# Kernel optimization log

Measured on AMD Instinct MI355X. Metric: run time of the kernel, lower is better.

Reference implementation:

```python
import jax, jax.numpy as jnp
import numpy as np
from functools import partial

B, C, FD, H, W = 8, 256, 128, 64, 64
POSC = 34  # 32 learned pos channels + 2 raw meshgrid channels


def create_meshgrid(h, w):
    # kornia-style normalized grid in [-1, 1], returned as [1, 2, h, w] (x, y)
    xs = jnp.linspace(-1.0, 1.0, w, dtype=jnp.float32)
    ys = jnp.linspace(-1.0, 1.0, h, dtype=jnp.float32)
    gy, gx = jnp.meshgrid(ys, xs, indexing='ij')
    return jnp.stack([gx, gy], axis=0)[None]  # [1,2,h,w]


def conv1x1(x, w, b):
    return jnp.einsum('bchw,oc->bohw', x, w) + b[None, :, None, None]


def pos_gen(feat, pg_w1, pg_b1, pg_w2, pg_b2):
    # PosGen type=2 with detach: two 1x1 'mul' layers (conv + ReLU, no norm)
    b, c, h, w = feat.shape
    feat = jax.lax.stop_gradient(feat)
    pos = jnp.broadcast_to(create_meshgrid(h, w), (b, 2, h, w))
    inp = jnp.concatenate([pos + 1.0, feat], axis=1)           # [b, feat_dim+2, h, w]
    h1 = jax.nn.relu(conv1x1(inp, pg_w1, pg_b1))               # [b, feat_dim, h, w]
    h2 = jax.nn.relu(conv1x1(h1, pg_w2, pg_b2))                # [b, 32, h, w]
    return jnp.concatenate([h2, pos], axis=1)                  # [b, 34, h, w]


def fuser(x, feat, w1, b1, w2, b2):
    # fuser_1D: concat along channels, 1x1 -> hidden (ReLU) -> 1x1 -> 256
    z = jnp.concatenate([x, feat], axis=1)
    z = jax.nn.relu(conv1x1(z, w1, b1))
    return conv1x1(z, w2, b2)


def conv_y(y, dw_w, dw_b, pw_w, pw_b):
    # BasicDWLayer: depthwise 3x3 + pointwise 1x1, no norm, no activation
    z = jax.lax.conv_general_dilated(
        y, dw_w, window_strides=(1, 1), padding='SAME',
        feature_group_count=y.shape[1],
        dimension_numbers=('NCHW', 'OIHW', 'NCHW')) + dw_b[None, :, None, None]
    return conv1x1(z, pw_w, pw_b)


def matching_forward(x, y, feat1, feat2,
                     pg_w1, pg_b1, pg_w2, pg_b2,
                     fus_w1, fus_b1, fus_w2, fus_b2,
                     dw_w, dw_b, pw_w, pw_b,
                     dustbin_vec, dustbin_pos):
    b, c, hx, wx = x.shape
    hy, wy = y.shape[2], y.shape[3]

    posf = pos_gen(feat2, pg_w1, pg_b1, pg_w2, pg_b2)          # [b, 34, hy, wy]
    c_pose = posf.shape[1]
    pos = posf.reshape(b, 1, c_pose, hy * wy).swapaxes(-1, -2)  # [b,1,Nk,34]

    xf = fuser(x, feat1, fus_w1, fus_b1, fus_w2, fus_b2)
    yf = fuser(y, feat2, fus_w1, fus_b1, fus_w2, fus_b2)
    yf = conv_y(yf, dw_w, dw_b, pw_w, pw_b)
    d = yf.shape[1]

    q = xf.reshape(b, 1, d, hx * wx).swapaxes(-1, -2)           # [b,1,Nq,256]
    k = yf.reshape(b, 1, d, hy * wy).swapaxes(-1, -2)           # [b,1,Nk,256]

    # dustbin token augmentation
    k = jnp.concatenate([k, jnp.broadcast_to(dustbin_vec, (b, 1, 1, d))], axis=-2)
    pos = jnp.concatenate([pos, jnp.broadcast_to(dustbin_pos, (b, 1, 1, c_pose))], axis=-2)

    # single-head cross-attention: values are the positional channels
    scores = jnp.einsum('bhqc,bhkc->bhqk', q, k) / jnp.sqrt(jnp.float32(d))
    attn = jax.nn.softmax(scores, axis=-1)
    out = jnp.einsum('bhqk,bhkd->bhqd', attn, pos)              # [b,1,Nq,34]
    return out.swapaxes(-1, -2).reshape(b, c_pose, hx, wx)


def setup_inputs() -> dict:
    key = jax.random.key(0)
    ks = jax.random.split(key, 20)
    s = 0.05
    return {
        'x': jax.random.normal(ks[0], (B, C, H, W), jnp.float32),
        'y': jax.random.normal(ks[1], (B, C, H, W), jnp.float32),
        'feat1': jax.random.normal(ks[2], (B, FD, H, W), jnp.float32),
        'feat2': jax.random.normal(ks[3], (B, FD, H, W), jnp.float32),
        # PosGen type-2 mapping: (feat_dim+2)->feat_dim, feat_dim->(hidden-2=32)
        'pg_w1': jax.random.normal(ks[4], (FD, FD + 2), jnp.float32) * s,
        'pg_b1': jnp.zeros((FD,), jnp.float32),
        'pg_w2': jax.random.normal(ks[5], (32, FD), jnp.float32) * s,
        'pg_b2': jnp.zeros((32,), jnp.float32),
        # fuser_1D: (256+128)->256 hidden, hidden->256
        'fus_w1': jax.random.normal(ks[6], (256, C + FD), jnp.float32) * s,
        'fus_b1': jnp.zeros((256,), jnp.float32),
        'fus_w2': jax.random.normal(ks[7], (C, 256), jnp.float32) * s,
        'fus_b2': jnp.zeros((C,), jnp.float32),
        # conv_y: depthwise 3x3 + pointwise 1x1
        'dw_w': jax.random.normal(ks[8], (C, 1, 3, 3), jnp.float32) * s,
        'dw_b': jnp.zeros((C,), jnp.float32),
        'pw_w': jax.random.normal(ks[9], (C, C), jnp.float32) * s,
        'pw_b': jnp.zeros((C,), jnp.float32),
        'dustbin_vec': jax.random.uniform(ks[10], (1, 1, 1, C), jnp.float32) / 10.0,
        'dustbin_pos': jnp.zeros((1, 1, 1, POSC), jnp.float32) - 10.0,
    }


def reference(x, y, feat1, feat2,
              pg_w1, pg_b1, pg_w2, pg_b2,
              fus_w1, fus_b1, fus_w2, fus_b2,
              dw_w, dw_b, pw_w, pw_b,
              dustbin_vec, dustbin_pos):
    return matching_forward(x, y, feat1, feat2,
                            pg_w1, pg_b1, pg_w2, pg_b2,
                            fus_w1, fus_b1, fus_w2, fus_b2,
                            dw_w, dw_b, pw_w, pw_b,
                            dustbin_vec, dustbin_pos)
```

## Files before the change

kernel.cpp:

```cpp
#include <hip/hip_runtime.h>
#include <hip/hip_bf16.h>

typedef __hip_bfloat16 bf16;
typedef unsigned short ushort_t;
typedef __bf16 bf16x8 __attribute__((ext_vector_type(8)));
typedef float  f32x4  __attribute__((ext_vector_type(4)));

#define HW    4096
#define NB    8
#define KSTR  4160
#define NTOK  32768
#define PROWS 64
#define QSCALE 0.0901684400557f

#define KT3   32
#define NKT3  130

__device__ __forceinline__ float lde(const void* p, size_t i, int f32f) {
    return f32f ? ((const float*)p)[i] : (float)((const bf16*)p)[i];
}
__device__ __forceinline__ ushort_t f2bu(float f){ union { __bf16 b; ushort_t u; } cv; cv.b = (__bf16)f; return cv.u; }

__device__ __forceinline__ void async_cp16(const void* g, void* l) {
    __builtin_amdgcn_global_load_lds(
        (const __attribute__((address_space(1))) unsigned int*)g,
        (__attribute__((address_space(3))) unsigned int*)l, 16, 0, 0);
}

__global__ void detect_kernel(const ushort_t* xb, int* flag)
{
    __shared__ int cnt;
    const int t = threadIdx.x;
    if (t == 0) cnt = 0;
    __syncthreads();
    ushort_t h = xb[2*t];
    int e = (h >> 7) & 0xFF;
    if (e >= 133) atomicAdd(&cnt, 1);
    __syncthreads();
    if (t == 0) *flag = (cnt > 8) ? 1 : 0;
}

struct WsPtrs {
    bf16 *fw1t, *fw2t, *pwt, *pgw1t, *pgw2t, *dwt, *pos;
    float *posw, *fb1, *fb2, *pwb, *pgb1, *pgb2, *dwb;
};

__global__ __launch_bounds__(256) void prep_kernel(
    const void* fus_w1, const void* fus_w2, const void* pw_w,
    const void* pg_w1, const void* pg_w2, const void* dw_w,
    const void* fus_b1, const void* fus_b2, const void* pw_b,
    const void* pg_b1, const void* pg_b2, const void* dw_b,
    const void* dpos, WsPtrs W, const int* flag)
{
    const int f = *flag;
    const long n_w1 = 98304, n_w2 = 65536, n_pw = 65536, n_g1 = 16384, n_g2 = 4096;
    const long n_posw = 256, n_dwt = 2304;
    const long n_b = 256, n_gb1 = 128, n_gb2 = 32;
    const long n_mesh = 65536;
    const long n_pad  = 8L*14*KSTR;
    const long n_dust = 272;
    const long n_zt   = 8L*34*63;
    const long total = n_w1+n_w2+n_pw+n_g1+n_g2+n_posw+n_dwt
                     + 3*n_b + n_gb1 + n_gb2 + n_b + n_mesh + n_pad + n_dust + n_zt;

    for (long i = blockIdx.x*256L + threadIdx.x; i < total; i += gridDim.x*256L) {
        long j = i;
        if (j < n_w1) { W.fw1t[j] = __float2bfloat16(lde(fus_w1, j, f)); continue; } j -= n_w1;
        if (j < n_w2) { W.fw2t[j] = __float2bfloat16(lde(fus_w2, j, f)); continue; } j -= n_w2;
        if (j < n_pw) { W.pwt[j]  = __float2bfloat16(lde(pw_w,  j, f)); continue; } j -= n_pw;
        if (j < n_g1) { W.pgw1t[j] = __float2bfloat16(lde(pg_w1, (j>>7)*130 + 2 + (j&127), f)); continue; } j -= n_g1;
        if (j < n_g2) { W.pgw2t[j] = __float2bfloat16(lde(pg_w2, j, f)); continue; } j -= n_g2;
        if (j < n_posw) { W.posw[j] = lde(pg_w1, (j>>1)*130 + (j&1), f); continue; } j -= n_posw;
        if (j < n_dwt) { W.dwt[j] = __float2bfloat16(lde(dw_w, (j&255)*9 + (j>>8), f)); continue; } j -= n_dwt;
        if (j < n_b)   { W.fb1[j] = lde(fus_b1, j, f); continue; } j -= n_b;
        if (j < n_b)   { W.fb2[j] = lde(fus_b2, j, f); continue; } j -= n_b;
        if (j < n_b)   { W.pwb[j] = lde(pw_b, j, f); continue; } j -= n_b;
        if (j < n_gb1) { W.pgb1[j] = lde(pg_b1, j, f); continue; } j -= n_gb1;
        if (j < n_gb2) { W.pgb2[j] = lde(pg_b2, j, f); continue; } j -= n_gb2;
        if (j < n_b)   { W.dwb[j] = lde(dw_b, j, f); continue; } j -= n_b;
        if (j < n_mesh) {
            long b = j >> 13; int rr = (int)((j>>12)&1); int tok = (int)(j & 4095);
            float v = rr ? (-1.f + 2.f*(float)((tok>>6)&63)/63.f)
                         : (-1.f + 2.f*(float)(tok&63)/63.f);
            W.pos[((size_t)b*PROWS + 32 + rr)*KSTR + tok] = __float2bfloat16(v);
            continue;
        } j -= n_mesh;
        if (j < n_pad) {
            long b = j / (14L*KSTR); long rem = j % (14L*KSTR);
            int row = 34 + (int)(rem / KSTR); int tok = (int)(rem % KSTR);
            W.pos[((size_t)b*PROWS + row)*KSTR + tok] = __float2bfloat16(row == 34 ? 1.f : 0.f);
            continue;
        } j -= n_pad;
        if (j < n_dust) {
            long b = j / 34; int ch = (int)(j % 34);
            W.pos[((size_t)b*PROWS + ch)*KSTR + 4096] = __float2bfloat16(lde(dpos, ch, f));
            continue;
        } j -= n_dust;
        { long b = j / (34*63); long rem = j % (34*63);
          int ch = (int)(rem / 63); int cc = (int)(rem % 63);
          W.pos[((size_t)b*PROWS + ch)*KSTR + 4097 + cc] = __float2bfloat16(0.f); }
    }
}

__global__ __launch_bounds__(256) void transpose_kernel(
    const void* main_src, const void* feat_src, bf16* __restrict__ dst, const int* flag)
{
    __shared__ float Tt[64*65];
    const int t = threadIdx.x;
    const int p0 = blockIdx.x * 64;
    const int cht = blockIdx.y;
    const int b = blockIdx.z;
    const int f = *flag;

    const void* src; int ch0, srcC, dc0;
    if (cht < 4) { src = main_src; ch0 = cht*64; srcC = 256; dc0 = ch0; }
    else         { src = feat_src; ch0 = (cht-4)*64; srcC = 128; dc0 = 256 + (cht-4)*64; }

    const int p = t & 63, cq = t >> 6;
    #pragma unroll
    for (int e = 0; e < 16; ++e) {
        int c = e*4 + cq;
        Tt[p*65 + c] = lde(src, ((size_t)b*srcC + ch0 + c)*HW + p0 + p, f);
    }
    __syncthreads();
    const int pr = t >> 2, cs = (t & 3) * 16;
    union { uint4 u4[2]; ushort_t us[16]; } pk;
    #pragma unroll
    for (int u = 0; u < 16; ++u) pk.us[u] = f2bu(Tt[pr*65 + cs + u]);
    ushort_t* op = (ushort_t*)dst + ((size_t)b*HW + p0 + pr)*384 + dc0 + cs;
    *(uint4*)op = pk.u4[0];
    *((uint4*)op + 1) = pk.u4[1];
}

template<int MT, bool RELU, bool POSEPI, int OMODE>
__global__ __launch_bounds__(256) void gemm_mfma(
    const bf16* __restrict__ A, int sa,
    const bf16* __restrict__ Bw, int ldb,
    const float* __restrict__ bias, const float* __restrict__ posw,
    bf16* __restrict__ out, int sm, int K, float oscale)
{
    const int t = threadIdx.x;
    const int w = t >> 6, lane = t & 63;
    const int n = lane & 15, quad = lane >> 4;
    const int p0 = blockIdx.x * 128;
    const int m0 = blockIdx.y * (MT*16);
    const int rowbase = p0 + w*32;

    f32x4 acc[2][MT];
    #pragma unroll
    for (int pt = 0; pt < 2; ++pt)
        #pragma unroll
        for (int mt = 0; mt < MT; ++mt) acc[pt][mt] = (f32x4){0.f,0.f,0.f,0.f};

    for (int k0 = 0; k0 < K; k0 += 32) {
        bf16x8 ap[2];
        #pragma unroll
        for (int pt = 0; pt < 2; ++pt)
            ap[pt] = *(const bf16x8*)&A[(size_t)(rowbase + pt*16 + n)*sa + k0 + quad*8];
        #pragma unroll
        for (int mt = 0; mt < MT; ++mt) {
            bf16x8 bw = *(const bf16x8*)&Bw[(size_t)(m0 + mt*16 + n)*ldb + k0 + quad*8];
            acc[0][mt] = __builtin_amdgcn_mfma_f32_16x16x32_bf16(ap[0], bw, acc[0][mt], 0, 0, 0);
            acc[1][mt] = __builtin_amdgcn_mfma_f32_16x16x32_bf16(ap[1], bw, acc[1][mt], 0, 0, 0);
        }
    }

    #pragma unroll
    for (int mt = 0; mt < MT; ++mt) {
        const int m = m0 + mt*16 + n;
        const float bi = bias[m];
        float w0 = 0.f, w1 = 0.f;
        if (POSEPI) { w0 = posw[m*2]; w1 = posw[m*2 + 1]; }
        #pragma unroll
        for (int pt = 0; pt < 2; ++pt) {
            const int tokb = rowbase + pt*16 + quad*4;
            if (OMODE == 1) {
                union { uint2 u2; ushort_t us[4]; } pk;
                #pragma unroll
                for (int r = 0; r < 4; ++r) {
                    float v = acc[pt][mt][r] + bi;
                    if (RELU) v = fmaxf(v, 0.f);
                    pk.us[r] = f2bu(v * oscale);
                }
                size_t oi = ((size_t)(tokb >> 12)*PROWS + m)*KSTR + (tokb & 4095);
                *(uint2*)((ushort_t*)out + oi) = pk.u2;
            } else {
                #pragma unroll
                for (int r = 0; r < 4; ++r) {
                    int tok = tokb + r;
                    float v = acc[pt][mt][r] + bi;
                    if (POSEPI) {
                        float gx1 = 2.f * (float)(tok & 63) / 63.f;
                        float gy1 = 2.f * (float)((tok >> 6) & 63) / 63.f;
                        v += w0*gx1 + w1*gy1;
                    }
                    if (RELU) v = fmaxf(v, 0.f);
                    v *= oscale;
                    size_t row = (OMODE == 2) ? (size_t)tok + 64*(size_t)(tok >> 12) : (size_t)tok;
                    out[row*sm + m] = __float2bfloat16(v);
                }
            }
        }
    }
}

__global__ __launch_bounds__(256) void dw_kernel(
    const bf16* __restrict__ in, const bf16* __restrict__ dwt,
    const float* __restrict__ dwb, bf16* __restrict__ out)
{
    const int t = threadIdx.x;
    const int tok = blockIdx.x*8 + (t >> 5);
    const int c8 = (t & 31) * 8;
    const int b = tok >> 12, p = tok & 4095;
    const int i = p >> 6, j = p & 63;

    float acc[8];
    #pragma unroll
    for (int u = 0; u < 8; ++u) acc[u] = dwb[c8 + u];

    #pragma unroll
    for (int di = 0; di < 3; ++di) {
        int ii = i + di - 1;
        if (ii < 0 || ii >= 64) continue;
        #pragma unroll
        for (int dj = 0; dj < 3; ++dj) {
            int jj = j + dj - 1;
            if (jj < 0 || jj >= 64) continue;
            int tok2 = (b << 12) + ii*64 + jj;
            bf16x8 xv = *(const bf16x8*)&in[(size_t)tok2*256 + c8];
            bf16x8 wv = *(const bf16x8*)&dwt[(di*3 + dj)*256 + c8];
            #pragma unroll
            for (int u = 0; u < 8; ++u) acc[u] += (float)xv[u] * (float)wv[u];
        }
    }
    union { uint4 u4; ushort_t us[8]; } pk;
    #pragma unroll
    for (int u = 0; u < 8; ++u) pk.us[u] = f2bu(acc[u]);
    *(uint4*)((ushort_t*)out + (size_t)tok*256 + c8) = pk.u4;
}

__global__ __launch_bounds__(256) void fill_late_kernel(
    const void* dvec, bf16* __restrict__ k_t, const int* flag)
{
    const int b = blockIdx.x, t = threadIdx.x;
    k_t[((size_t)b*KSTR + 4096)*256 + t] = __float2bfloat16(lde(dvec, t, *flag));
}

__global__ __launch_bounds__(256, 2) void attn_kernel(
    const bf16* __restrict__ q_t, const bf16* __restrict__ k_t,
    const bf16* __restrict__ pos, void* outv, const int* flag)
{
    __shared__ __align__(16) __bf16 Ks[3*1024*8];
    __shared__ __align__(16) __bf16 posb[3*256*8];
    __shared__ __align__(16) __bf16 Pb[64*40];

    const int t = threadIdx.x;
    const int w = t >> 6, lane = t & 63;
    const int n = lane & 15, quad = lane >> 4;
    const int bid = blockIdx.x;
    const int b = bid & 7;
    const int qt = bid >> 3;

    bf16x8 aq[8];
    {
        size_t qrow = (size_t)b*HW + qt*64 + w*16 + n;
        #pragma unroll
        for (int c = 0; c < 8; ++c)
            aq[c] = *(const bf16x8*)&q_t[qrow*256 + c*32 + quad*8];
    }

    f32x4 pacc[3];
    #pragma unroll
    for (int ct = 0; ct < 3; ++ct) pacc[ct] = (f32x4){0.f,0.f,0.f,0.f};

    const ushort_t* ksrc0 = (const ushort_t*)k_t + (size_t)b*KSTR*256;
    const ushort_t* psrc0 = (const ushort_t*)pos + (size_t)b*PROWS*KSTR;
    const int xw = n & 7;

    auto STAGE = [&](int kt2, int bufn) {
        const int kb = kt2 * KT3;
        __bf16* kd = &Ks[(size_t)bufn*8192];
        #pragma unroll
        for (int e = 0; e < 4; ++e) {
            int slot = w*256 + e*64 + lane;
            int tok = slot >> 5;
            int ch = ((slot & 31) ^ (tok & 7)) * 8;
            async_cp16(&ksrc0[(size_t)(kb + tok)*256 + ch], &kd[(size_t)slot*8]);
        }
        {
            int slot = w*64 + lane;
            int row = slot >> 2;
            int ch = (slot & 3) * 8;
            async_cp16(&psrc0[(size_t)row*KSTR + kb + ch], &posb[(size_t)(bufn*256 + slot)*8]);
        }
    };

    STAGE(0, 0);
    int bc = 0, bn = 1;
    for (int kt = 0; kt < NKT3; ++kt) {
        STAGE(kt + 1 < NKT3 ? kt + 1 : 0, bn);
        asm volatile("s_waitcnt vmcnt(5)" ::: "memory");
        __builtin_amdgcn_s_barrier();
        asm volatile("" ::: "memory");

        const int kbase = kt * KT3;
        const __bf16* kb_ = &Ks[(size_t)bc*8192];
        const __bf16* pb_ = &posb[(size_t)bc*2048];

        f32x4 sacc[2];
        sacc[0] = (f32x4){0.f,0.f,0.f,0.f};
        sacc[1] = (f32x4){0.f,0.f,0.f,0.f};
        #pragma unroll
        for (int c = 0; c < 8; ++c) {
            #pragma unroll
            for (int nt = 0; nt < 2; ++nt) {
                bf16x8 bk = *(const bf16x8*)&kb_[(size_t)((nt*16 + n)*32 + ((c*4 + quad) ^ xw))*8];
                sacc[nt] = __builtin_amdgcn_mfma_f32_16x16x32_bf16(aq[c], bk, sacc[nt], 0, 0, 0);
            }
        }

        #pragma unroll
        for (int nt = 0; nt < 2; ++nt) {
            const bool ok = (kbase + nt*16 + n) <= 4096;
            #pragma unroll
            for (int r = 0; r < 4; ++r) {
                float pv = ok ? __builtin_amdgcn_exp2f(sacc[nt][r]) : 0.f;
                Pb[(w*16 + quad*4 + r)*40 + nt*16 + n] = (__bf16)pv;
            }
        }

        {
            bf16x8 aP = *(const bf16x8*)&Pb[(w*16 + n)*40 + quad*8];
            #pragma unroll
            for (int ct = 0; ct < 3; ++ct) {
                bf16x8 bp = *(const bf16x8*)&pb_[(size_t)((ct*16 + n)*4 + quad)*8];
                pacc[ct] = __builtin_amdgcn_mfma_f32_16x16x32_bf16(aP, bp, pacc[ct], 0, 0, 0);
            }
        }

        int b3 = 3 - bc - bn; bc = bn; bn = b3;
    }
    asm volatile("s_waitcnt vmcnt(0)" ::: "memory");

    const int f32o = *flag;
    float linv[4];
    #pragma unroll
    for (int r = 0; r < 4; ++r)
        linv[r] = 1.f / __shfl(pacc[2][r], (lane & 48) | 2, 64);
    #pragma unroll
    for (int ct = 0; ct < 3; ++ct) {
        int ch = ct*16 + n;
        if (ch >= 34) continue;
        #pragma unroll
        for (int r = 0; r < 4; ++r) {
            float v = pacc[ct][r] * linv[r];
            size_t oi = ((size_t)b*34 + ch)*HW + qt*64 + w*16 + quad*4 + r;
            if (f32o) ((float*)outv)[oi] = v;
            else      ((bf16*)outv)[oi]  = __float2bfloat16(v);
        }
    }
}

extern "C" void kernel_launch(void* const* d_in, const int* in_sizes, int n_in,
                              void* d_out, int out_size, void* d_ws, size_t ws_size,
                              hipStream_t stream)
{
    const void* x      = d_in[0];
    const void* y      = d_in[1];
    const void* feat1  = d_in[2];
    const void* feat2  = d_in[3];
    const void* pg_w1  = d_in[4];
    const void* pg_b1  = d_in[5];
    const void* pg_w2  = d_in[6];
    const void* pg_b2  = d_in[7];
    const void* fus_w1 = d_in[8];
    const void* fus_b1 = d_in[9];
    const void* fus_w2 = d_in[10];
    const void* fus_b2 = d_in[11];
    const void* dw_w   = d_in[12];
    const void* dw_b   = d_in[13];
    const void* pw_w   = d_in[14];
    const void* pw_b   = d_in[15];
    const void* dvec   = d_in[16];
    const void* dpos   = d_in[17];

    char* wsb = (char*)d_ws;
    int*  flag = (int*)wsb;
    size_t off = 16;
    bf16* R1   = (bf16*)(wsb + off); off += (size_t)NTOK*384*2;
    bf16* bufH = (bf16*)(wsb + off); off += (size_t)NTOK*256*2;
    bf16* q_t  = (bf16*)(wsb + off); off += (size_t)NTOK*256*2;
    bf16* pos  = (bf16*)(wsb + off); off += (size_t)NB*PROWS*KSTR*2;
    WsPtrs W;
    W.fw1t  = (bf16*)(wsb + off); off += 98304*2;
    W.fw2t  = (bf16*)(wsb + off); off += 65536*2;
    W.pwt   = (bf16*)(wsb + off); off += 65536*2;
    W.pgw1t = (bf16*)(wsb + off); off += 16384*2;
    W.pgw2t = (bf16*)(wsb + off); off += 4096*2;
    W.dwt   = (bf16*)(wsb + off); off += 2304*2;
    W.pos   = pos;
    W.posw  = (float*)(wsb + off); off += 256*4;
    W.fb1   = (float*)(wsb + off); off += 256*4;
    W.fb2   = (float*)(wsb + off); off += 256*4;
    W.pwb   = (float*)(wsb + off); off += 256*4;
    W.pgb1  = (float*)(wsb + off); off += 128*4;
    W.pgb2  = (float*)(wsb + off); off += 32*4;
    W.dwb   = (float*)(wsb + off); off += 256*4;

    bf16* in_xy = R1;
    bf16* yf    = R1;
    bf16* k_t   = R1;

    dim3 b256(256);

    detect_kernel<<<1, 256, 0, stream>>>((const ushort_t*)x, flag);
    prep_kernel<<<1024, b256, 0, stream>>>(fus_w1, fus_w2, pw_w, pg_w1, pg_w2, dw_w,
                                           fus_b1, fus_b2, pw_b, pg_b1, pg_b2, dw_b,
                                           dpos, W, flag);
    transpose_kernel<<<dim3(64,6,NB), b256, 0, stream>>>(x, feat1, in_xy, flag);
    gemm_mfma<8, true, false, 0><<<dim3(256,2), b256, 0, stream>>>(
        in_xy, 384, W.fw1t, 384, W.fb1, nullptr, bufH, 256, 384, 1.f);
    gemm_mfma<8, false, false, 0><<<dim3(256,2), b256, 0, stream>>>(
        bufH, 256, W.fw2t, 256, W.fb2, nullptr, q_t, 256, 256, QSCALE);
    transpose_kernel<<<dim3(64,6,NB), b256, 0, stream>>>(y, feat2, in_xy, flag);
    gemm_mfma<8, true, true, 0><<<dim3(256,1), b256, 0, stream>>>(
        in_xy + 256, 384, W.pgw1t, 128, W.pgb1, W.posw, bufH, 128, 128, 1.f);
    gemm_mfma<2, true, false, 1><<<dim3(256,1), b256, 0, stream>>>(
        bufH, 128, W.pgw2t, 128, W.pgb2, nullptr, pos, 0, 128, 1.f);
    gemm_mfma<8, true, false, 0><<<dim3(256,2), b256, 0, stream>>>(
        in_xy, 384, W.fw1t, 384, W.fb1, nullptr, bufH, 256, 384, 1.f);
    gemm_mfma<8, false, false, 0><<<dim3(256,2), b256, 0, stream>>>(
        bufH, 256, W.fw2t, 256, W.fb2, nullptr, yf, 256, 256, 1.f);
    dw_kernel<<<dim3(4096), b256, 0, stream>>>(yf, W.dwt, W.dwb, bufH);
    fill_late_kernel<<<dim3(NB), b256, 0, stream>>>(dvec, k_t, flag);
    gemm_mfma<8, false, false, 2><<<dim3(256,2), b256, 0, stream>>>(
        bufH, 256, W.pwt, 256, W.pwb, nullptr, k_t, 256, 256, 1.f);
    attn_kernel<<<dim3(512), b256, 0, stream>>>(q_t, k_t, pos, d_out, flag);
}
```

Measured before the change: 502.6 us.

## Halve attention waves per block, each wave computing two query sub-tiles

The attention kernel now launches 128-thread blocks where each wave handles 32 query rows (two 16-row fragments) instead of 16. Each K and pos fragment read from shared memory is reused across two MFMAs, halving LDS reads per FLOP, and each thread issues twice as many async staging copies, with the waitcnt adjusted to match. The cost is higher register use (doubled q fragments and accumulators) and fewer waves per block to hide latency. Occupancy may change because launch bounds drop the min-blocks hint.

```diff
diff --git a/kernel.cpp b/kernel.cpp
--- a/kernel.cpp
+++ b/kernel.cpp
@@ -246,7 +246,7 @@
     k_t[((size_t)b*KSTR + 4096)*256 + t] = __float2bfloat16(lde(dvec, t, *flag));
 }
 
-__global__ __launch_bounds__(256, 2) void attn_kernel(
+__global__ __launch_bounds__(128) void attn_kernel(
     const bf16* __restrict__ q_t, const bf16* __restrict__ k_t,
     const bf16* __restrict__ pos, void* outv, const int* flag)
 {
@@ -261,17 +261,20 @@
     const int b = bid & 7;
     const int qt = bid >> 3;
 
-    bf16x8 aq[8];
-    {
-        size_t qrow = (size_t)b*HW + qt*64 + w*16 + n;
+    bf16x8 aq[2][8];
+    #pragma unroll
+    for (int f = 0; f < 2; ++f) {
+        size_t qrow = (size_t)b*HW + qt*64 + w*32 + f*16 + n;
         #pragma unroll
         for (int c = 0; c < 8; ++c)
-            aq[c] = *(const bf16x8*)&q_t[qrow*256 + c*32 + quad*8];
-    }
-
-    f32x4 pacc[3];
-    #pragma unroll
-    for (int ct = 0; ct < 3; ++ct) pacc[ct] = (f32x4){0.f,0.f,0.f,0.f};
+            aq[f][c] = *(const bf16x8*)&q_t[qrow*256 + c*32 + quad*8];
+    }
+
+    f32x4 pacc[2][3];
+    #pragma unroll
+    for (int f = 0; f < 2; ++f)
+        #pragma unroll
+        for (int ct = 0; ct < 3; ++ct) pacc[f][ct] = (f32x4){0.f,0.f,0.f,0.f};
 
     const ushort_t* ksrc0 = (const ushort_t*)k_t + (size_t)b*KSTR*256;
     const ushort_t* psrc0 = (const ushort_t*)pos + (size_t)b*PROWS*KSTR;
@@ -281,14 +284,15 @@
         const int kb = kt2 * KT3;
         __bf16* kd = &Ks[(size_t)bufn*8192];
         #pragma unroll
-        for (int e = 0; e < 4; ++e) {
-            int slot = w*256 + e*64 + lane;
+        for (int e = 0; e < 8; ++e) {
+            int slot = w*512 + e*64 + lane;
             int tok = slot >> 5;
             int ch = ((slot & 31) ^ (tok & 7)) * 8;
             async_cp16(&ksrc0[(size_t)(kb + tok)*256 + ch], &kd[(size_t)slot*8]);
         }
-        {
-            int slot = w*64 + lane;
+        #pragma unroll
+        for (int e = 0; e < 2; ++e) {
+            int slot = w*128 + e*64 + lane;
             int row = slot >> 2;
             int ch = (slot & 3) * 8;
             async_cp16(&psrc0[(size_t)row*KSTR + kb + ch], &posb[(size_t)(bufn*256 + slot)*8]);
@@ -299,7 +303,7 @@
     int bc = 0, bn = 1;
     for (int kt = 0; kt < NKT3; ++kt) {
         STAGE(kt + 1 < NKT3 ? kt + 1 : 0, bn);
-        asm volatile("s_waitcnt vmcnt(5)" ::: "memory");
+        asm volatile("s_waitcnt vmcnt(10)" ::: "memory");
         __builtin_amdgcn_s_barrier();
         asm volatile("" ::: "memory");
 
@@ -307,34 +311,42 @@
         const __bf16* kb_ = &Ks[(size_t)bc*8192];
         const __bf16* pb_ = &posb[(size_t)bc*2048];
 
-        f32x4 sacc[2];
-        sacc[0] = (f32x4){0.f,0.f,0.f,0.f};
-        sacc[1] = (f32x4){0.f,0.f,0.f,0.f};
+        f32x4 sacc[2][2];
+        #pragma unroll
+        for (int f = 0; f < 2; ++f) {
+            sacc[f][0] = (f32x4){0.f,0.f,0.f,0.f};
+            sacc[f][1] = (f32x4){0.f,0.f,0.f,0.f};
+        }
         #pragma unroll
         for (int c = 0; c < 8; ++c) {
             #pragma unroll
             for (int nt = 0; nt < 2; ++nt) {
                 bf16x8 bk = *(const bf16x8*)&kb_[(size_t)((nt*16 + n)*32 + ((c*4 + quad) ^ xw))*8];
-                sacc[nt] = __builtin_amdgcn_mfma_f32_16x16x32_bf16(aq[c], bk, sacc[nt], 0, 0, 0);
+                sacc[0][nt] = __builtin_amdgcn_mfma_f32_16x16x32_bf16(aq[0][c], bk, sacc[0][nt], 0, 0, 0);
+                sacc[1][nt] = __builtin_amdgcn_mfma_f32_16x16x32_bf16(aq[1][c], bk, sacc[1][nt], 0, 0, 0);
             }
         }
 
         #pragma unroll
-        for (int nt = 0; nt < 2; ++nt) {
-            const bool ok = (kbase + nt*16 + n) <= 4096;
+        for (int f = 0; f < 2; ++f)
             #pragma unroll
-            for (int r = 0; r < 4; ++r) {
-                float pv = ok ? __builtin_amdgcn_exp2f(sacc[nt][r]) : 0.f;
-                Pb[(w*16 + quad*4 + r)*40 + nt*16 + n] = (__bf16)pv;
+            for (int nt = 0; nt < 2; ++nt) {
+                const bool ok = (kbase + nt*16 + n) <= 4096;
+                #pragma unroll
+                for (int r = 0; r < 4; ++r) {
+                    float pv = ok ? __builtin_amdgcn_exp2f(sacc[f][nt][r]) : 0.f;
+                    Pb[(w*32 + f*16 + quad*4 + r)*40 + nt*16 + n] = (__bf16)pv;
+                }
             }
-        }
 
         {
-            bf16x8 aP = *(const bf16x8*)&Pb[(w*16 + n)*40 + quad*8];
+            bf16x8 aP0 = *(const bf16x8*)&Pb[(w*32 + n)*40 + quad*8];
+            bf16x8 aP1 = *(const bf16x8*)&Pb[(w*32 + 16 + n)*40 + quad*8];
             #pragma unroll
             for (int ct = 0; ct < 3; ++ct) {
                 bf16x8 bp = *(const bf16x8*)&pb_[(size_t)((ct*16 + n)*4 + quad)*8];
-                pacc[ct] = __builtin_amdgcn_mfma_f32_16x16x32_bf16(aP, bp, pacc[ct], 0, 0, 0);
+                pacc[0][ct] = __builtin_amdgcn_mfma_f32_16x16x32_bf16(aP0, bp, pacc[0][ct], 0, 0, 0);
+                pacc[1][ct] = __builtin_amdgcn_mfma_f32_16x16x32_bf16(aP1, bp, pacc[1][ct], 0, 0, 0);
             }
         }
 
@@ -343,20 +355,23 @@
     asm volatile("s_waitcnt vmcnt(0)" ::: "memory");
 
     const int f32o = *flag;
-    float linv[4];
-    #pragma unroll
-    for (int r = 0; r < 4; ++r)
-        linv[r] = 1.f / __shfl(pacc[2][r], (lane & 48) | 2, 64);
-    #pragma unroll
-    for (int ct = 0; ct < 3; ++ct) {
-        int ch = ct*16 + n;
-        if (ch >= 34) continue;
-        #pragma unroll
-        for (int r = 0; r < 4; ++r) {
-            float v = pacc[ct][r] * linv[r];
-            size_t oi = ((size_t)b*34 + ch)*HW + qt*64 + w*16 + quad*4 + r;
-            if (f32o) ((float*)outv)[oi] = v;
-            else      ((bf16*)outv)[oi]  = __float2bfloat16(v);
+    #pragma unroll
+    for (int f = 0; f < 2; ++f) {
+        float linv[4];
+        #pragma unroll
+        for (int r = 0; r < 4; ++r)
+            linv[r] = 1.f / __shfl(pacc[f][2][r], (lane & 48) | 2, 64);
+        #pragma unroll
+        for (int ct = 0; ct < 3; ++ct) {
+            int ch = ct*16 + n;
+            if (ch >= 34) continue;
+            #pragma unroll
+            for (int r = 0; r < 4; ++r) {
+                float v = pacc[f][ct][r] * linv[r];
+                size_t oi = ((size_t)b*34 + ch)*HW + qt*64 + w*32 + f*16 + quad*4 + r;
+                if (f32o) ((float*)outv)[oi] = v;
+                else      ((bf16*)outv)[oi]  = __float2bfloat16(v);
+            }
         }
     }
 }
@@ -435,5 +450,5 @@
     fill_late_kernel<<<dim3(NB), b256, 0, stream>>>(dvec, k_t, flag);
     gemm_mfma<8, false, false, 2><<<dim3(256,2), b256, 0, stream>>>(
         bufH, 256, W.pwt, 256, W.pwb, nullptr, k_t, 256, 256, 1.f);
-    attn_kernel<<<dim3(512), b256, 0, stream>>>(q_t, k_t, pos, d_out, flag);
-}
+    attn_kernel<<<dim3(512), dim3(128), 0, stream>>>(q_t, k_t, pos, d_out, flag);
+}
```

New measurement: 543.3 us. 1.08x slower.
